# Kernel optimization log

Measured on AMD Instinct MI355X. Metric: run time of the kernel, lower is better.

Reference implementation:

```python
import jax, jax.numpy as jnp
import numpy as np
from collections import deque

N = 768          # number of nodes (x.shape[0])
DEG = 8          # out-degree of the random directed graph
E = N * DEG      # number of edges
H = 32           # head_num
MAX_ENTRIES = 10_000_000  # fixed COO size (pad with zero coeff)
MAX_PATHS = 3    # original truncates all_shortest_paths to first 3


def _build_graph_coeffs():
    """Replicates the networkx all_shortest_paths logic exactly, emitting a
    flat COO list: out[i,j] += coeff * enc[node] with
    coeff = 1 / (len(path) * num_paths_ij), num_paths_ij <= 3."""
    rng = np.random.default_rng(0)
    src = rng.integers(0, N, E)
    dst = rng.integers(0, N, E)
    adj = [[] for _ in range(N)]
    for u, v in zip(src.tolist(), dst.tolist()):
        if u != v:  # self-loops never appear on a shortest path
            adj[u].append(v)
    pair_l, node_l, coeff_l = [], [], []
    for i in range(N):
        # BFS from i, recording shortest-path predecessor DAG
        dist = [-1] * N
        pred = [None] * N
        dist[i] = 0
        q = deque([i])
        while q:
            u = q.popleft()
            du1 = dist[u] + 1
            for v in adj[u]:
                if dist[v] == -1:
                    dist[v] = du1
                    pred[v] = [u]
                    q.append(v)
                elif dist[v] == du1:
                    pred[v].append(u)
        base = i * N
        for j in range(N):
            if dist[j] == -1:
                continue  # unreachable -> out[i,j] stays 0 (the `except: continue`)
            # enumerate up to MAX_PATHS shortest paths via predecessor DAG
            paths = []
            stack = [(j, (j,))]
            while stack and len(paths) < MAX_PATHS:
                v, path = stack.pop()
                if v == i:
                    paths.append(path)
                    continue
                for u in pred[v]:
                    stack.append((u, path + (u,)))
            k = len(paths)
            pij = base + j
            for path in paths:
                c = 1.0 / (len(path) * k)  # per-path node mean, then mean over paths
                for n in path:
                    pair_l.append(pij)
                    node_l.append(n)
                    coeff_l.append(c)
    pair = np.asarray(pair_l, dtype=np.int32)
    node = np.asarray(node_l, dtype=np.int32)
    coeff = np.asarray(coeff_l, dtype=np.float32)
    m = pair.shape[0]
    if m > MAX_ENTRIES:
        pair, node, coeff = pair[:MAX_ENTRIES], node[:MAX_ENTRIES], coeff[:MAX_ENTRIES]
    else:
        pad = MAX_ENTRIES - m
        pair = np.concatenate([pair, np.zeros(pad, np.int32)])
        node = np.concatenate([node, np.zeros(pad, np.int32)])
        coeff = np.concatenate([coeff, np.zeros(pad, np.float32)])
    return src, dst, pair, node, coeff


def setup_inputs() -> dict:
    key = jax.random.key(0)
    k1, k2, k3, k4 = jax.random.split(key, 4)
    src, dst, pair, node, coeff = _build_graph_coeffs()
    bound = 1.0 / np.sqrt(4.0)  # nn.Linear(4, H) default init range
    return {
        "x": jax.random.normal(k1, (N, 128), jnp.float32),
        "edge_attr": jax.random.normal(k2, (N, 4), jnp.float32),
        "W": jax.random.uniform(k3, (H, 4), jnp.float32, -bound, bound),
        "b": jax.random.uniform(k4, (H,), jnp.float32, -bound, bound),
        "edge_idx": jnp.asarray(np.stack([src, dst]).astype(np.int64)),
        "pair_idx": jnp.asarray(pair),
        "node_idx": jnp.asarray(node),
        "coeff": jnp.asarray(coeff),
        "num_nodes": N,
    }


def reference(x, edge_attr, W, b, edge_idx, pair_idx, node_idx, coeff, num_nodes):
    n = num_nodes
    enc = edge_attr @ W.T + b                      # [N, H] edge_encoder per node
    vals = coeff[:, None] * enc[node_idx]          # [M, H] weighted gather
    out = jax.ops.segment_sum(vals, pair_idx, num_segments=n * n)  # [N*N, H]
    return out.reshape(n, n, -1).transpose(2, 0, 1)  # 'h w n -> n h w'
```

## Files before the change

### kernel.cpp

```cpp
#include <hip/hip_runtime.h>

#define N2 (768 * 768)
#define NH 32
#define PPB 64
#define TPB 256
#define CAP 1664

typedef float v4f __attribute__((ext_vector_type(4)));

__global__ void bounds_kernel(const int* __restrict__ pair,
                              const float* __restrict__ coeff,
                              int* __restrict__ bnd, int M) {
    int j = blockIdx.x * blockDim.x + threadIdx.x;
    if (j > N2 / PPB) return;
    int target = j * PPB;
    int lo = 0, hi = M;
    while (lo < hi) {
        int mid = (lo + hi) >> 1;
        int key = (coeff[mid] == 0.f) ? 0x7fffffff : pair[mid];
        if (key < target) lo = mid + 1; else hi = mid;
    }
    bnd[j] = lo;
}

__global__ __launch_bounds__(256) void fused_kernel(
    const int* __restrict__ pair, const int* __restrict__ node,
    const float* __restrict__ coeff, const float* __restrict__ ea,
    const float* __restrict__ W, const float* __restrict__ bias,
    const int* __restrict__ bnd, float* __restrict__ out, int M)
{
    __shared__ float2 ent[CAP];
    __shared__ float sum[5][PPB];
    __shared__ int ps[PPB], pe[PPB];
    __shared__ float sW[NH * 4];
    __shared__ float sBias[NH];

    const int t = threadIdx.x;
    const int p0 = blockIdx.x * PPB;

    if (t < NH * 4) sW[t] = W[t];
    if (t < NH) sBias[t] = bias[t];
    if (t < PPB) { ps[t] = 0; pe[t] = 0; }
    __syncthreads();

    const int s0 = bnd[blockIdx.x], s1 = bnd[blockIdx.x + 1];
    const int s0a = s0 & ~3;
    const int cntA = s1 - s0a;
    const bool staged = (cntA <= CAP);

    if (staged) {
        for (int i4 = t; (i4 << 2) < cntA; i4 += TPB) {
            const int e0 = s0a + (i4 << 2);
            const int4   p4 = reinterpret_cast<const int4*>(pair)[e0 >> 2];
            const int4   n4 = reinterpret_cast<const int4*>(node)[e0 >> 2];
            const float4 c4 = reinterpret_cast<const float4*>(coeff)[e0 >> 2];
            v4f w0; w0.x = c4.x; w0.y = __int_as_float(n4.x);
                    w0.z = c4.y; w0.w = __int_as_float(n4.y);
            v4f w1; w1.x = c4.z; w1.y = __int_as_float(n4.z);
                    w1.z = c4.w; w1.w = __int_as_float(n4.w);
            *reinterpret_cast<v4f*>(&ent[i4 << 2])       = w0;
            *reinterpret_cast<v4f*>(&ent[(i4 << 2) + 2]) = w1;
            const int prevp = (e0 > 0) ? pair[e0 - 1] : -1;
            const int nextp = (e0 + 4 < M) ? pair[e0 + 4] : -1;
            const int pk[6] = { prevp, p4.x, p4.y, p4.z, p4.w, nextp };
#pragma unroll
            for (int j = 0; j < 4; ++j) {
                const int e = e0 + j;
                const int pp = pk[j + 1];
                if (e >= s0 && e < s1) {
                    if (e == s0 || pk[j] != pp) ps[pp - p0] = e;
                    if (e == s1 - 1 || pk[j + 2] != pp) pe[pp - p0] = e + 1;
                }
            }
        }
    } else {
        const int cnt = s1 - s0;
        for (int i = t; i < cnt; i += TPB) {
            int e = s0 + i;
            int pp = pair[e];
            if (i == 0 || pair[e - 1] != pp) ps[pp - p0] = e;
            if (i == cnt - 1 || pair[e + 1] != pp) pe[pp - p0] = e + 1;
        }
    }
    __syncthreads();

    const int q = t >> 2, sub = t & 3;
    float a0 = 0.f, a1 = 0.f, a2 = 0.f, a3 = 0.f, a4 = 0.f;
    float b0s = 0.f, b1s = 0.f, b2s = 0.f, b3s = 0.f, b4s = 0.f;
    {
        const int e = pe[q];
        int k = ps[q] + (sub << 1);
        if (staged) {
            for (; k < e; k += 8) {
                const float2 enA = ent[k - s0a];
                const float ccA = enA.x;
                const int ndA = __float_as_int(enA.y);
                const float4 vA = *reinterpret_cast<const float4*>(ea + ndA * 4);
                a0 += ccA; a1 += ccA * vA.x; a2 += ccA * vA.y; a3 += ccA * vA.z; a4 += ccA * vA.w;
                if (k + 1 < e) {
                    const float2 enB = ent[k + 1 - s0a];
                    const float ccB = enB.x;
                    const int ndB = __float_as_int(enB.y);
                    const float4 vB = *reinterpret_cast<const float4*>(ea + ndB * 4);
                    b0s += ccB; b1s += ccB * vB.x; b2s += ccB * vB.y; b3s += ccB * vB.z; b4s += ccB * vB.w;
                }
            }
        } else {
            for (; k < e; k += 8) {
                const float ccA = coeff[k];
                const float4 vA = *reinterpret_cast<const float4*>(ea + node[k] * 4);
                a0 += ccA; a1 += ccA * vA.x; a2 += ccA * vA.y; a3 += ccA * vA.z; a4 += ccA * vA.w;
                if (k + 1 < e) {
                    const float ccB = coeff[k + 1];
                    const float4 vB = *reinterpret_cast<const float4*>(ea + node[k + 1] * 4);
                    b0s += ccB; b1s += ccB * vB.x; b2s += ccB * vB.y; b3s += ccB * vB.z; b4s += ccB * vB.w;
                }
            }
        }
    }
    a0 += b0s; a1 += b1s; a2 += b2s; a3 += b3s; a4 += b4s;
#pragma unroll
    for (int d = 1; d < 4; d <<= 1) {
        a0 += __shfl_xor(a0, d); a1 += __shfl_xor(a1, d); a2 += __shfl_xor(a2, d);
        a3 += __shfl_xor(a3, d); a4 += __shfl_xor(a4, d);
    }
    if (sub == 0) {
        sum[0][q] = a0; sum[1][q] = a1; sum[2][q] = a2;
        sum[3][q] = a3; sum[4][q] = a4;
    }
    __syncthreads();

    {
        const int l = t & 63, w = t >> 6;
        const int g = l & 15, quad = l >> 4;
        const v4f c0 = *reinterpret_cast<const v4f*>(&sum[0][4 * g]);
        const v4f c1 = *reinterpret_cast<const v4f*>(&sum[1][4 * g]);
        const v4f c2 = *reinterpret_cast<const v4f*>(&sum[2][4 * g]);
        const v4f c3 = *reinterpret_cast<const v4f*>(&sum[3][4 * g]);
        const v4f c4 = *reinterpret_cast<const v4f*>(&sum[4][4 * g]);
        const size_t op = (size_t)p0 + 4 * g;
#pragma unroll
        for (int j = 0; j < 2; ++j) {
            const int h = w * 8 + quad * 2 + j;
            const float bb = sBias[h], w0 = sW[h * 4], w1 = sW[h * 4 + 1],
                        w2 = sW[h * 4 + 2], w3 = sW[h * 4 + 3];
            v4f o = bb * c0 + w0 * c1 + w1 * c2 + w2 * c3 + w3 * c4;
            __builtin_nontemporal_store(o, reinterpret_cast<v4f*>(out + (size_t)h * N2 + op));
        }
    }
}

extern "C" void kernel_launch(void* const* d_in, const int* in_sizes, int n_in,
                              void* d_out, int out_size, void* d_ws, size_t ws_size,
                              hipStream_t stream) {
    const float* ea    = (const float*)d_in[1];
    const float* W     = (const float*)d_in[2];
    const float* b     = (const float*)d_in[3];
    const int*   pair  = (const int*)d_in[5];
    const int*   node  = (const int*)d_in[6];
    const float* coeff = (const float*)d_in[7];
    float* out = (float*)d_out;
    int M = in_sizes[5];

    int* bnd = (int*)d_ws;

    bounds_kernel<<<(N2 / PPB + 1 + 255) / 256, 256, 0, stream>>>(pair, coeff, bnd, M);

    fused_kernel<<<N2 / PPB, TPB, 0, stream>>>(pair, node, coeff, ea, W, b, bnd, out, M);
}
```

Before: 48.21 us.

## Make each wavefront process its own 16-pair segment without block barriers

Each 64-lane wavefront now owns an independent 16-pair tile, with its own staging buffer, segment bounds and reduction scratch. All __syncthreads barriers are removed, so wavefronts no longer wait on each other. W and bias are read straight from global memory instead of being copied into shared memory. The bounds kernel now does four times as many binary searches, and the unstaged fallback switches to per-pair binary searches. Wave-level LDS visibility without explicit barriers is assumed to be safe; it relies on the hardware running all 64 lanes of a wavefront in lockstep.

```diff
diff --git a/kernel.cpp b/kernel.cpp
--- a/kernel.cpp
+++ b/kernel.cpp
@@ -2,9 +2,10 @@
 
 #define N2 (768 * 768)
 #define NH 32
-#define PPB 64
+#define PPW 16
+#define WPB 4
 #define TPB 256
-#define CAP 1664
+#define CAPW 512
 
 typedef float v4f __attribute__((ext_vector_type(4)));
 
@@ -12,8 +13,8 @@
                               const float* __restrict__ coeff,
                               int* __restrict__ bnd, int M) {
     int j = blockIdx.x * blockDim.x + threadIdx.x;
-    if (j > N2 / PPB) return;
-    int target = j * PPB;
+    if (j > N2 / PPW) return;
+    int target = j * PPW;
     int lo = 0, hi = M;
     while (lo < hi) {
         int mid = (lo + hi) >> 1;
@@ -29,37 +30,34 @@
     const float* __restrict__ W, const float* __restrict__ bias,
     const int* __restrict__ bnd, float* __restrict__ out, int M)
 {
-    __shared__ float2 ent[CAP];
-    __shared__ float sum[5][PPB];
-    __shared__ int ps[PPB], pe[PPB];
-    __shared__ float sW[NH * 4];
-    __shared__ float sBias[NH];
+    __shared__ float2 ent[WPB][CAPW];
+    __shared__ int ps[WPB][PPW], pe[WPB][PPW];
+    __shared__ float sum[WPB][5][PPW];
 
     const int t = threadIdx.x;
-    const int p0 = blockIdx.x * PPB;
+    const int w = t >> 6, lane = t & 63;
+    const int wv = blockIdx.x * WPB + w;
+    const int p0 = wv * PPW;
 
-    if (t < NH * 4) sW[t] = W[t];
-    if (t < NH) sBias[t] = bias[t];
-    if (t < PPB) { ps[t] = 0; pe[t] = 0; }
-    __syncthreads();
+    if (lane < PPW) { ps[w][lane] = 0; pe[w][lane] = 0; }
 
-    const int s0 = bnd[blockIdx.x], s1 = bnd[blockIdx.x + 1];
+    const int s0 = bnd[wv], s1 = bnd[wv + 1];
     const int s0a = s0 & ~3;
     const int cntA = s1 - s0a;
-    const bool staged = (cntA <= CAP);
+    const bool staged = (cntA <= CAPW);
 
     if (staged) {
-        for (int i4 = t; (i4 << 2) < cntA; i4 += TPB) {
+        for (int i4 = lane; (i4 << 2) < cntA; i4 += 64) {
             const int e0 = s0a + (i4 << 2);
             const int4   p4 = reinterpret_cast<const int4*>(pair)[e0 >> 2];
             const int4   n4 = reinterpret_cast<const int4*>(node)[e0 >> 2];
             const float4 c4 = reinterpret_cast<const float4*>(coeff)[e0 >> 2];
-            v4f w0; w0.x = c4.x; w0.y = __int_as_float(n4.x);
-                    w0.z = c4.y; w0.w = __int_as_float(n4.y);
-            v4f w1; w1.x = c4.z; w1.y = __int_as_float(n4.z);
-                    w1.z = c4.w; w1.w = __int_as_float(n4.w);
-            *reinterpret_cast<v4f*>(&ent[i4 << 2])       = w0;
-            *reinterpret_cast<v4f*>(&ent[(i4 << 2) + 2]) = w1;
+            v4f w0v; w0v.x = c4.x; w0v.y = __int_as_float(n4.x);
+                     w0v.z = c4.y; w0v.w = __int_as_float(n4.y);
+            v4f w1v; w1v.x = c4.z; w1v.y = __int_as_float(n4.z);
+                     w1v.z = c4.w; w1v.w = __int_as_float(n4.w);
+            *reinterpret_cast<v4f*>(&ent[w][i4 << 2])       = w0v;
+            *reinterpret_cast<v4f*>(&ent[w][(i4 << 2) + 2]) = w1v;
             const int prevp = (e0 > 0) ? pair[e0 - 1] : -1;
             const int nextp = (e0 + 4 < M) ? pair[e0 + 4] : -1;
             const int pk[6] = { prevp, p4.x, p4.y, p4.z, p4.w, nextp };
@@ -68,53 +66,45 @@
                 const int e = e0 + j;
                 const int pp = pk[j + 1];
                 if (e >= s0 && e < s1) {
-                    if (e == s0 || pk[j] != pp) ps[pp - p0] = e;
-                    if (e == s1 - 1 || pk[j + 2] != pp) pe[pp - p0] = e + 1;
+                    if (e == s0 || pk[j] != pp) ps[w][pp - p0] = e - s0a;
+                    if (e == s1 - 1 || pk[j + 2] != pp) pe[w][pp - p0] = e - s0a + 1;
                 }
             }
         }
-    } else {
-        const int cnt = s1 - s0;
-        for (int i = t; i < cnt; i += TPB) {
-            int e = s0 + i;
-            int pp = pair[e];
-            if (i == 0 || pair[e - 1] != pp) ps[pp - p0] = e;
-            if (i == cnt - 1 || pair[e + 1] != pp) pe[pp - p0] = e + 1;
-        }
     }
-    __syncthreads();
 
-    const int q = t >> 2, sub = t & 3;
+    const int q = lane >> 2, sub = lane & 3;
     float a0 = 0.f, a1 = 0.f, a2 = 0.f, a3 = 0.f, a4 = 0.f;
     float b0s = 0.f, b1s = 0.f, b2s = 0.f, b3s = 0.f, b4s = 0.f;
-    {
-        const int e = pe[q];
-        int k = ps[q] + (sub << 1);
-        if (staged) {
-            for (; k < e; k += 8) {
-                const float2 enA = ent[k - s0a];
-                const float ccA = enA.x;
-                const int ndA = __float_as_int(enA.y);
-                const float4 vA = *reinterpret_cast<const float4*>(ea + ndA * 4);
-                a0 += ccA; a1 += ccA * vA.x; a2 += ccA * vA.y; a3 += ccA * vA.z; a4 += ccA * vA.w;
-                if (k + 1 < e) {
-                    const float2 enB = ent[k + 1 - s0a];
-                    const float ccB = enB.x;
-                    const int ndB = __float_as_int(enB.y);
-                    const float4 vB = *reinterpret_cast<const float4*>(ea + ndB * 4);
-                    b0s += ccB; b1s += ccB * vB.x; b2s += ccB * vB.y; b3s += ccB * vB.z; b4s += ccB * vB.w;
-                }
+    if (staged) {
+        const int e = pe[w][q];
+        int k = ps[w][q] + (sub << 1);
+        for (; k < e; k += 8) {
+            const float2 enA = ent[w][k];
+            const float ccA = enA.x;
+            const float4 vA = *reinterpret_cast<const float4*>(ea + __float_as_int(enA.y) * 4);
+            a0 += ccA; a1 += ccA * vA.x; a2 += ccA * vA.y; a3 += ccA * vA.z; a4 += ccA * vA.w;
+            if (k + 1 < e) {
+                const float2 enB = ent[w][k + 1];
+                const float ccB = enB.x;
+                const float4 vB = *reinterpret_cast<const float4*>(ea + __float_as_int(enB.y) * 4);
+                b0s += ccB; b1s += ccB * vB.x; b2s += ccB * vB.y; b3s += ccB * vB.z; b4s += ccB * vB.w;
             }
-        } else {
-            for (; k < e; k += 8) {
-                const float ccA = coeff[k];
-                const float4 vA = *reinterpret_cast<const float4*>(ea + node[k] * 4);
-                a0 += ccA; a1 += ccA * vA.x; a2 += ccA * vA.y; a3 += ccA * vA.z; a4 += ccA * vA.w;
-                if (k + 1 < e) {
-                    const float ccB = coeff[k + 1];
-                    const float4 vB = *reinterpret_cast<const float4*>(ea + node[k + 1] * 4);
-                    b0s += ccB; b1s += ccB * vB.x; b2s += ccB * vB.y; b3s += ccB * vB.z; b4s += ccB * vB.w;
-                }
+        }
+    } else {
+        const int tgt = p0 + q;
+        int lo = s0, hi = s1;
+        while (lo < hi) { int mid = (lo + hi) >> 1; if (pair[mid] < tgt) lo = mid + 1; else hi = mid; }
+        const int st = lo; hi = s1;
+        while (lo < hi) { int mid = (lo + hi) >> 1; if (pair[mid] <= tgt) lo = mid + 1; else hi = mid; }
+        for (int k = st + (sub << 1); k < lo; k += 8) {
+            const float ccA = coeff[k];
+            const float4 vA = *reinterpret_cast<const float4*>(ea + node[k] * 4);
+            a0 += ccA; a1 += ccA * vA.x; a2 += ccA * vA.y; a3 += ccA * vA.z; a4 += ccA * vA.w;
+            if (k + 1 < lo) {
+                const float ccB = coeff[k + 1];
+                const float4 vB = *reinterpret_cast<const float4*>(ea + node[k + 1] * 4);
+                b0s += ccB; b1s += ccB * vB.x; b2s += ccB * vB.y; b3s += ccB * vB.z; b4s += ccB * vB.w;
             }
         }
     }
@@ -125,26 +115,24 @@
         a3 += __shfl_xor(a3, d); a4 += __shfl_xor(a4, d);
     }
     if (sub == 0) {
-        sum[0][q] = a0; sum[1][q] = a1; sum[2][q] = a2;
-        sum[3][q] = a3; sum[4][q] = a4;
+        sum[w][0][q] = a0; sum[w][1][q] = a1; sum[w][2][q] = a2;
+        sum[w][3][q] = a3; sum[w][4][q] = a4;
     }
-    __syncthreads();
 
     {
-        const int l = t & 63, w = t >> 6;
-        const int g = l & 15, quad = l >> 4;
-        const v4f c0 = *reinterpret_cast<const v4f*>(&sum[0][4 * g]);
-        const v4f c1 = *reinterpret_cast<const v4f*>(&sum[1][4 * g]);
-        const v4f c2 = *reinterpret_cast<const v4f*>(&sum[2][4 * g]);
-        const v4f c3 = *reinterpret_cast<const v4f*>(&sum[3][4 * g]);
-        const v4f c4 = *reinterpret_cast<const v4f*>(&sum[4][4 * g]);
+        const int g = lane & 3, hh = lane >> 2;
+        const v4f c0 = *reinterpret_cast<const v4f*>(&sum[w][0][4 * g]);
+        const v4f c1 = *reinterpret_cast<const v4f*>(&sum[w][1][4 * g]);
+        const v4f c2 = *reinterpret_cast<const v4f*>(&sum[w][2][4 * g]);
+        const v4f c3 = *reinterpret_cast<const v4f*>(&sum[w][3][4 * g]);
+        const v4f c4v = *reinterpret_cast<const v4f*>(&sum[w][4][4 * g]);
         const size_t op = (size_t)p0 + 4 * g;
 #pragma unroll
         for (int j = 0; j < 2; ++j) {
-            const int h = w * 8 + quad * 2 + j;
-            const float bb = sBias[h], w0 = sW[h * 4], w1 = sW[h * 4 + 1],
-                        w2 = sW[h * 4 + 2], w3 = sW[h * 4 + 3];
-            v4f o = bb * c0 + w0 * c1 + w1 * c2 + w2 * c3 + w3 * c4;
+            const int h = hh + j * 16;
+            const float4 wr = *reinterpret_cast<const float4*>(W + h * 4);
+            const float bb = bias[h];
+            v4f o = bb * c0 + wr.x * c1 + wr.y * c2 + wr.z * c3 + wr.w * c4v;
             __builtin_nontemporal_store(o, reinterpret_cast<v4f*>(out + (size_t)h * N2 + op));
         }
     }
@@ -164,7 +152,7 @@
 
     int* bnd = (int*)d_ws;
 
-    bounds_kernel<<<(N2 / PPB + 1 + 255) / 256, 256, 0, stream>>>(pair, coeff, bnd, M);
+    bounds_kernel<<<(N2 / PPW + 1 + 255) / 256, 256, 0, stream>>>(pair, coeff, bnd, M);
 
-    fused_kernel<<<N2 / PPB, TPB, 0, stream>>>(pair, node, coeff, ea, W, b, bnd, out, M);
+    fused_kernel<<<N2 / (PPW * WPB), TPB, 0, stream>>>(pair, node, coeff, ea, W, b, bnd, out, M);
 }
```

New measurement: 49.10 us. No clear change (+1.9%).
